# Kernel optimization log

Hardware: AMD Instinct MI355X
Metric: run time of the kernel (lower is better)

## Reference

```python
import jax, jax.numpy as jnp
import numpy as np

N_RAYS = 16384
MAX_HITS = 16
S_PER_VOX = 4          # samples per intersected voxel
N_VOX = 524288         # voxel embedding table size
D_VOX = 16             # voxel feature dim
HID = 64               # sdf/rgb MLP hidden dim
FEAT = 15              # geometry feature dim passed to rgb net
BETA = 0.1             # VolSDF-style laplace/logistic density sharpness


def setup_inputs() -> dict:
    key = jax.random.key(0)
    ks = jax.random.split(key, 12)
    rays_o = jax.random.normal(ks[0], (N_RAYS, 3), dtype=jnp.float32)
    rd = jax.random.normal(ks[1], (N_RAYS, 3), dtype=jnp.float32)
    rays_d = rd / jnp.linalg.norm(rd, axis=-1, keepdims=True)
    raw = jax.random.randint(ks[2], (N_RAYS, MAX_HITS), 0, 2 * N_VOX)
    vox_idx = jnp.where(raw < N_VOX, raw, -1)
    t0 = jnp.sort(jax.random.uniform(ks[3], (N_RAYS, MAX_HITS), minval=0.5, maxval=6.0), axis=-1)
    seg = jax.random.uniform(ks[4], (N_RAYS, MAX_HITS), minval=0.02, maxval=0.2)
    t_near, t_far = t0, t0 + seg
    ray_hits = jnp.any(vox_idx >= 0, axis=-1)
    s = 0.1
    embed_table = jax.random.normal(ks[5], (N_VOX, D_VOX), dtype=jnp.float32) * s
    W1 = jax.random.normal(ks[6], (3 + D_VOX, HID), dtype=jnp.float32) * s
    b1 = jnp.zeros((HID,), jnp.float32)
    W2 = jax.random.normal(ks[7], (HID, 1 + FEAT), dtype=jnp.float32) * s
    b2 = jnp.zeros((1 + FEAT,), jnp.float32)
    Wr1 = jax.random.normal(ks[8], (3 + FEAT, HID), dtype=jnp.float32) * s
    br1 = jnp.zeros((HID,), jnp.float32)
    Wr2 = jax.random.normal(ks[9], (HID, 3), dtype=jnp.float32) * s
    br2 = jnp.zeros((3,), jnp.float32)
    return dict(rays_o=rays_o, rays_d=rays_d, vox_idx=vox_idx, t_near=t_near,
                t_far=t_far, ray_hits=ray_hits, embed_table=embed_table,
                W1=W1, b1=b1, W2=W2, b2=b2, Wr1=Wr1, br1=br1, Wr2=Wr2, br2=br2)


def reference(rays_o, rays_d, vox_idx, t_near, t_far, ray_hits,
              embed_table, W1, b1, W2, b2, Wr1, br1, Wr2, br2):
    N = rays_o.shape[0]
    M = MAX_HITS * S_PER_VOX  # max_samples per ray
    # ---- point_sampler: S_PER_VOX uniform midpoints inside each hit voxel ----
    frac = (jnp.arange(S_PER_VOX, dtype=jnp.float32) + 0.5) / S_PER_VOX  # [S]
    seg = t_far - t_near                                                  # [N,H]
    t_vals = (t_near[..., None] + seg[..., None] * frac).reshape(N, M)    # [N,M]
    dists = jnp.broadcast_to((seg / S_PER_VOX)[..., None],
                             (N, MAX_HITS, S_PER_VOX)).reshape(N, M)      # [N,M]
    p2v_idx = jnp.broadcast_to(vox_idx[..., None],
                               (N, MAX_HITS, S_PER_VOX)).reshape(N, M)    # [N,M]
    mask_pts = p2v_idx >= 0                                               # [N,M]
    pts = rays_o[:, None, :] + t_vals[..., None] * rays_d[:, None, :]     # [N,M,3]
    # ---- voxel_embedder: gather voxel features (safe-index the misses) ----
    safe_idx = jnp.where(mask_pts, p2v_idx, 0)
    vox_embeds = embed_table[safe_idx]                                    # [N,M,Dv]
    # ---- sdf_net: 2-layer MLP -> sdf (1) + geometry feats (FEAT) ----
    x = jnp.concatenate([pts, vox_embeds], axis=-1)
    h = jax.nn.relu(jnp.einsum('nmi,ih->nmh', x, W1) + b1)
    so = jnp.einsum('nmh,ho->nmo', h, W2) + b2
    sdf = so[..., 0]                                                      # [N,M]
    feats = so[..., 1:]                                                   # [N,M,FEAT]
    # ---- rgb_net on (view dir, feats) ----
    rdir = jnp.broadcast_to(rays_d[:, None, :], (N, M, 3))
    xr = jnp.concatenate([rdir, feats], axis=-1)
    hr = jax.nn.relu(jnp.einsum('nmi,ih->nmh', xr, Wr1) + br1)
    rgb = jax.nn.sigmoid(jnp.einsum('nmh,ho->nmo', hr, Wr2) + br2)        # [N,M,3]
    # ---- density_fn + masked_scatter (invalid points -> 0) ----
    density = (1.0 / BETA) * jax.nn.sigmoid(-sdf / BETA)
    mf = mask_pts.astype(rgb.dtype)
    free_energy = density * dists * mf                                    # [N,M]
    rgb = rgb * mf[..., None]
    sdf_sc = sdf * mf
    # ---- volumetric_rendering_sdf ----
    alpha = 1.0 - jnp.exp(-free_energy)
    shifted = jnp.concatenate([jnp.zeros_like(free_energy[:, :1]),
                               jnp.cumsum(free_energy, axis=-1)[:, :-1]], axis=-1)
    T = jnp.exp(-shifted)
    weights = alpha * T                                                   # [N,M]
    rgb_map = jnp.einsum('nm,nmc->nc', weights, rgb)                      # [N,3]
    depth = jnp.sum(weights * t_vals, axis=-1)
    acc = jnp.sum(weights, axis=-1)
    eps = 1e-10
    disp = 1.0 / jnp.maximum(eps, depth / jnp.maximum(acc, eps))
    # ---- fill_in for rays with no hits (eval path) ----
    hm = ray_hits
    rgb_map = jnp.where(hm[:, None], rgb_map, 0.0)
    depth = jnp.where(hm, depth, 0.0)
    disp = jnp.where(hm, disp, 1000.0)
    acc = jnp.where(hm, acc, 0.0)
    weights = jnp.where(hm[:, None], weights, 0.0)
    sdf_out = jnp.where(hm[:, None], sdf_sc, 1.0)
    return rgb_map, depth, disp, acc, weights, sdf_out
```

## Files before the change

### kernel.cpp

```cpp
#include <hip/hip_runtime.h>

#define NRAYS  16384
#define WPB    4
#define GRID   4096

typedef _Float16 f16x2 __attribute__((ext_vector_type(2)));
typedef _Float16 f16x4 __attribute__((ext_vector_type(4)));
typedef _Float16 f16x8 __attribute__((ext_vector_type(8)));
typedef float    f32x4 __attribute__((ext_vector_type(4)));

static __device__ __forceinline__ f16x2 pk(float a, float b) {
    return __builtin_bit_cast(f16x2, __builtin_amdgcn_cvt_pkrtz(a, b));
}
static __device__ __forceinline__ f16x4 cat2(f16x2 lo, f16x2 hi) {
    return __builtin_shufflevector(lo, hi, 0, 1, 2, 3);
}
static __device__ __forceinline__ f16x4 pack4relu(f32x4 v) {
    f16x4 p = cat2(pk(v[0], v[1]), pk(v[2], v[3]));
    return __builtin_elementwise_max(p, (f16x4){});
}
template <int CTRL, int RMASK>
static __device__ __forceinline__ float dppadd(float x) {
    int t = __builtin_amdgcn_update_dpp(0, __builtin_bit_cast(int, x), CTRL, RMASK, 0xf, true);
    return x + __builtin_bit_cast(float, t);
}
static __device__ __forceinline__ float wavescan(float x) {
    x = dppadd<0x111, 0xf>(x);
    x = dppadd<0x112, 0xf>(x);
    x = dppadd<0x114, 0xf>(x);
    x = dppadd<0x118, 0xf>(x);
    x = dppadd<0x142, 0xa>(x);
    x = dppadd<0x143, 0xc>(x);
    return x;
}
static __device__ __forceinline__ float lane63(float x) {
    return __builtin_bit_cast(float, __builtin_amdgcn_readlane(__builtin_bit_cast(int, x), 63));
}
static __device__ __forceinline__ _Float16* rowp(_Float16* b, int row, int ch) {
    return b + (row << 5) + ((ch ^ (row & 3)) << 3);
}

#define MFMA32(a, b, c) __builtin_amdgcn_mfma_f32_16x16x32_f16(a, b, c, 0, 0, 0)
#define MFMA16(a, b, c) __builtin_amdgcn_mfma_f32_16x16x16f16(a, b, c, 0, 0, 0)

extern "C" __global__ void prep_frags(
    const float* __restrict__ W1, const float* __restrict__ b1,
    const float* __restrict__ W2, const float* __restrict__ b2,
    const float* __restrict__ Wr1, const float* __restrict__ br1,
    const float* __restrict__ Wr2, const float* __restrict__ br2,
    void* __restrict__ ws)
{
    _Float16* wsh = (_Float16*)ws;
    float*    wsf = (float*)ws;
    const int b = blockIdx.x;
    const int tid = threadIdx.x;
    const int l = tid & 63, g = tid >> 6;
    const int c = l & 15, q = l >> 4;
    if (b == 0) {
        const int m = g;
        #pragma unroll
        for (int e = 0; e < 8; ++e) {
            const int k = q * 8 + e;
            const float v = (k < 19) ? W1[k * 64 + m * 16 + c]
                                     : (k == 19 ? b1[m * 16 + c] : 0.f);
            wsh[(m * 64 + l) * 8 + e] = (_Float16)v;
        }
    } else if (b == 1) {
        const int mh = g;
        #pragma unroll
        for (int e = 0; e < 4; ++e) {
            wsh[2048 + (mh * 64 + l) * 4 + e] = (_Float16)W2[(mh * 16 + q * 4 + e) * 16 + c];
            wsh[5120 + (mh * 64 + l) * 4 + e] =
                (c < 3) ? (_Float16)Wr2[(mh * 16 + q * 4 + e) * 3 + c] : (_Float16)0.f;
        }
    } else if (b == 2) {
        const int mh = g;
        #pragma unroll
        for (int ks = 0; ks < 2; ++ks)
            #pragma unroll
            for (int e = 0; e < 4; ++e) {
                const int k = ks * 16 + q * 4 + e;
                const float v = (k < 18) ? Wr1[k * 64 + mh * 16 + c]
                                         : (k == 18 ? br1[mh * 16 + c] : 0.f);
                wsh[3072 + ((mh * 2 + ks) * 64 + l) * 4 + e] = (_Float16)v;
            }
    } else {
        if (g == 0) {
            #pragma unroll
            for (int j = 0; j < 4; ++j) wsf[3072 + l * 4 + j] = b2[q * 4 + j];
        } else if (g == 1) {
            #pragma unroll
            for (int j = 0; j < 4; ++j)
                wsf[3328 + l * 4 + j] = ((q * 4 + j) < 3) ? br2[q * 4 + j] : 0.f;
        }
    }
}

extern "C" __global__ __launch_bounds__(256, 4) void nerf_render_mfma(
    const float* __restrict__ rays_o,
    const float* __restrict__ rays_d,
    const int*   __restrict__ vox_idx,
    const float* __restrict__ t_near,
    const float* __restrict__ t_far,
    const float* __restrict__ embed,
    const void*  __restrict__ ws,
    float* __restrict__ out)
{
    __shared__ __align__(16) _Float16 buf_all[WPB][64 * 32];
    __shared__ __align__(16) f32x4    hof_all[WPB][64];
    __shared__ float                  sdf_all[WPB][64];

    const _Float16* frag  = (const _Float16*)ws;
    const float*    fragf = (const float*)ws;

    const int lane = threadIdx.x & 63;
    const int wv   = threadIdx.x >> 6;
    _Float16* buf = buf_all[wv];
    f32x4* hof = hof_all[wv];
    float* sdfb = sdf_all[wv];

    const int c  = lane & 15;
    const int q  = lane >> 4;
    const bool q0 = (q == 0);
    const int hh = lane >> 2, ss = lane & 3;
    const int bpaddr = ((lane + 48) & 63) << 2;

    const int ray = blockIdx.x * WPB + wv;

    const int   vi_raw = vox_idx[ray * 16 + hh];
    const float tn  = t_near[ray * 16 + hh];
    const float tfv = t_far [ray * 16 + hh];
    const float ox = rays_o[ray*3+0], oy = rays_o[ray*3+1], oz = rays_o[ray*3+2];
    const float dx = rays_d[ray*3+0], dy = rays_d[ray*3+1], dz = rays_d[ray*3+2];
    const int vi0 = vi_raw >= 0 ? vi_raw : 0;
    const float4* er = reinterpret_cast<const float4*>(embed + (long long)vi0 * 16);
    const float4 e0 = er[0], e1 = er[1], e2 = er[2], e3 = er[3];

    *(f16x8*)rowp(buf, lane, 3) = (f16x8){};

    const bool  mask = vi_raw >= 0;
    const float seg  = tfv - tn;
    const float t    = fmaf(seg, ((float)ss + 0.5f) * 0.25f, tn);
    const float dist = seg * 0.25f;
    const float p0 = fmaf(t, dx, ox), p1 = fmaf(t, dy, oy), p2 = fmaf(t, dz, oz);

    f16x8 r0 = {(_Float16)p0,   (_Float16)p1,   (_Float16)p2,   (_Float16)e0.x,
                (_Float16)e0.y, (_Float16)e0.z, (_Float16)e0.w, (_Float16)e1.x};
    f16x8 r1 = {(_Float16)e1.y, (_Float16)e1.z, (_Float16)e1.w, (_Float16)e2.x,
                (_Float16)e2.y, (_Float16)e2.z, (_Float16)e2.w, (_Float16)e3.x};
    f16x8 r2 = {(_Float16)e3.y, (_Float16)e3.z, (_Float16)e3.w, (_Float16)1.0f,
                (_Float16)0.0f, (_Float16)0.0f, (_Float16)0.0f, (_Float16)0.0f};
    *(f16x8*)rowp(buf, lane, 0) = r0;
    *(f16x8*)rowp(buf, lane, 1) = r1;
    *(f16x8*)rowp(buf, lane, 2) = r2;

    f16x8 bx[4];
    #pragma unroll
    for (int n = 0; n < 4; ++n)
        bx[n] = *(const f16x8*)rowp(buf, n * 16 + c, q);

    const f32x4 b2v = *(const f32x4*)(fragf + 3072 + lane * 4);
    f32x4 acc2[4];
    #pragma unroll
    for (int n = 0; n < 4; ++n) acc2[n] = b2v;
    #pragma unroll 1
    for (int m = 0; m < 4; ++m) {
        const f16x8 w1f = *(const f16x8*)(frag + (m * 64 + lane) * 8);
        const f16x4 w2a = *(const f16x4*)(frag + 2048 + (m * 64 + lane) * 4);
        #pragma unroll
        for (int np = 0; np < 2; ++np) {
            f32x4 a1[2] = {};
            #pragma unroll
            for (int i = 0; i < 2; ++i) a1[i] = MFMA32(w1f, bx[np * 2 + i], a1[i]);
            #pragma unroll
            for (int i = 0; i < 2; ++i) {
                const f16x4 hb = pack4relu(a1[i]);
                acc2[np * 2 + i] = MFMA16(w2a, hb, acc2[np * 2 + i]);
            }
        }
    }

    float sdfv[4]; f16x2 d0[4], d1[4]; int bd[4];
    #pragma unroll
    for (int n = 0; n < 4; ++n) {
        sdfv[n] = acc2[n][0];
        d0[n] = pk(acc2[n][0], acc2[n][1]);
        d1[n] = pk(acc2[n][2], acc2[n][3]);
    }
    #pragma unroll
    for (int n = 0; n < 4; ++n)
        bd[n] = __builtin_amdgcn_ds_bpermute(bpaddr, __builtin_bit_cast(int, d1[n]));

    if (q0) {
        #pragma unroll
        for (int n = 0; n < 4; ++n) sdfb[n * 16 + c] = sdfv[n];
    }

    const f16x2 dir01 = pk(dx, dy);
    const _Float16 dzh = (_Float16)dz;
    const f16x2 zero2 = {};
    const f16x2 onezero = {(_Float16)1.0f, (_Float16)0.0f};
    f16x4 bfr0[4], bfr1[4];
    #pragma unroll
    for (int n = 0; n < 4; ++n) {
        f16x2 bdn = __builtin_bit_cast(f16x2, bd[n]);
        f16x2 lo0 = q0 ? dir01 : bdn;
        f16x2 hi0 = q0 ? (f16x2){dzh, d0[n][1]} : d0[n];
        bfr0[n] = cat2(lo0, hi0);
        f16x2 lo1 = q0 ? bdn : zero2;
        f16x2 hi1 = q0 ? onezero : zero2;
        bfr1[n] = cat2(lo1, hi1);
    }

    float* out_rgb   = out;
    float* out_depth = out + NRAYS * 3;
    float* out_disp  = out_depth + NRAYS;
    float* out_acc   = out_disp + NRAYS;
    float* out_w     = out_acc + NRAYS;
    float* out_sdf   = out_w + NRAYS * 64;

    const float sdfs = sdfb[lane];
    const float mf = mask ? 1.0f : 0.0f;
    const float density = 10.0f / (1.0f + __expf(10.0f * sdfs));
    const float fe      = density * dist * mf;
    const float sdf_sc  = sdfs * mf;

    const float cum   = wavescan(fe);
    const float T     = __expf(fe - cum);
    const float alpha = 1.0f - __expf(-fe);
    const float w     = alpha * T;

    const float swt = lane63(wavescan(w * t));
    const float swa = lane63(wavescan(w));

    const bool hm = (__ballot((int)mask) != 0ull);

    out_w  [ray * 64 + lane] = hm ? w      : 0.0f;
    out_sdf[ray * 64 + lane] = hm ? sdf_sc : 1.0f;
    if (lane == 0) {
        if (hm) {
            out_depth[ray] = swt;
            out_acc[ray]   = swa;
            const float dd = swt / fmaxf(swa, 1e-10f);
            out_disp[ray]  = 1.0f / fmaxf(1e-10f, dd);
        } else {
            out_depth[ray] = 0.0f;
            out_acc[ray]   = 0.0f;
            out_disp[ray]  = 1000.0f;
        }
    }

    const f32x4 br2v = *(const f32x4*)(fragf + 3328 + lane * 4);
    f32x4 acc4[4];
    #pragma unroll
    for (int n = 0; n < 4; ++n) acc4[n] = br2v;
    #pragma unroll 1
    for (int mh = 0; mh < 4; ++mh) {
        const f16x4 wa0 = *(const f16x4*)(frag + 3072 + ((mh * 2 + 0) * 64 + lane) * 4);
        const f16x4 wa1 = *(const f16x4*)(frag + 3072 + ((mh * 2 + 1) * 64 + lane) * 4);
        const f16x4 w4  = *(const f16x4*)(frag + 5120 + (mh * 64 + lane) * 4);
        #pragma unroll
        for (int np = 0; np < 2; ++np) {
            f32x4 a3[2] = {};
            #pragma unroll
            for (int i = 0; i < 2; ++i) a3[i] = MFMA16(wa0, bfr0[np * 2 + i], a3[i]);
            #pragma unroll
            for (int i = 0; i < 2; ++i) a3[i] = MFMA16(wa1, bfr1[np * 2 + i], a3[i]);
            #pragma unroll
            for (int i = 0; i < 2; ++i) {
                const f16x4 hr = pack4relu(a3[i]);
                acc4[np * 2 + i] = MFMA16(w4, hr, acc4[np * 2 + i]);
            }
        }
    }

    if (q0) {
        #pragma unroll
        for (int n = 0; n < 4; ++n) {
            f32x4 o4 = {acc4[n][0], acc4[n][1], acc4[n][2], 0.0f};
            hof[n * 16 + c] = o4;
        }
    }
    const f32x4 mine = hof[lane];

    const float rr = mf / (1.0f + __expf(-mine[0]));
    const float gg = mf / (1.0f + __expf(-mine[1]));
    const float bb = mf / (1.0f + __expf(-mine[2]));

    const float swr = lane63(wavescan(w * rr));
    const float swg = lane63(wavescan(w * gg));
    const float swb = lane63(wavescan(w * bb));

    if (lane == 0) {
        if (hm) {
            out_rgb[ray * 3 + 0] = swr;
            out_rgb[ray * 3 + 1] = swg;
            out_rgb[ray * 3 + 2] = swb;
        } else {
            out_rgb[ray * 3 + 0] = 0.0f;
            out_rgb[ray * 3 + 1] = 0.0f;
            out_rgb[ray * 3 + 2] = 0.0f;
        }
    }
}

extern "C" void kernel_launch(void* const* d_in, const int* in_sizes, int n_in,
                              void* d_out, int out_size, void* d_ws, size_t ws_size,
                              hipStream_t stream) {
    const float* rays_o = (const float*)d_in[0];
    const float* rays_d = (const float*)d_in[1];
    const int*   vox    = (const int*)  d_in[2];
    const float* t_near = (const float*)d_in[3];
    const float* t_far  = (const float*)d_in[4];
    const float* embed  = (const float*)d_in[6];
    const float* W1  = (const float*)d_in[7];
    const float* b1  = (const float*)d_in[8];
    const float* W2  = (const float*)d_in[9];
    const float* b2  = (const float*)d_in[10];
    const float* Wr1 = (const float*)d_in[11];
    const float* br1 = (const float*)d_in[12];
    const float* Wr2 = (const float*)d_in[13];
    const float* br2 = (const float*)d_in[14];
    float* outp = (float*)d_out;

    prep_frags<<<dim3(4), dim3(256), 0, stream>>>(W1, b1, W2, b2, Wr1, br1, Wr2, br2, d_ws);
    nerf_render_mfma<<<dim3(GRID), dim3(256), 0, stream>>>(rays_o, rays_d, vox, t_near, t_far,
                                                           embed, d_ws, outp);
}
```

Measured before the change: 31.40 us.

## Split MLP passes into half-batches and alias LDS to double occupancy

```diff
diff --git a/kernel.cpp b/kernel.cpp
--- a/kernel.cpp
+++ b/kernel.cpp
@@ -96,7 +96,7 @@
     }
 }
 
-extern "C" __global__ __launch_bounds__(256, 4) void nerf_render_mfma(
+extern "C" __global__ __launch_bounds__(256, 8) void nerf_render_mfma(
     const float* __restrict__ rays_o,
     const float* __restrict__ rays_d,
     const int*   __restrict__ vox_idx,
@@ -107,8 +107,6 @@
     float* __restrict__ out)
 {
     __shared__ __align__(16) _Float16 buf_all[WPB][64 * 32];
-    __shared__ __align__(16) f32x4    hof_all[WPB][64];
-    __shared__ float                  sdf_all[WPB][64];
 
     const _Float16* frag  = (const _Float16*)ws;
     const float*    fragf = (const float*)ws;
@@ -116,8 +114,8 @@
     const int lane = threadIdx.x & 63;
     const int wv   = threadIdx.x >> 6;
     _Float16* buf = buf_all[wv];
-    f32x4* hof = hof_all[wv];
-    float* sdfb = sdf_all[wv];
+    f32x4* hof  = reinterpret_cast<f32x4*>(buf);
+    float* sdfb = reinterpret_cast<float*>(buf + 512);
 
     const int c  = lane & 15;
     const int q  = lane >> 4;
@@ -143,6 +141,9 @@
     const float t    = fmaf(seg, ((float)ss + 0.5f) * 0.25f, tn);
     const float dist = seg * 0.25f;
     const float p0 = fmaf(t, dx, ox), p1 = fmaf(t, dy, oy), p2 = fmaf(t, dz, oz);
+
+    const f16x2 dir01 = pk(dx, dy);
+    const _Float16 dzh = (_Float16)dz;
 
     f16x8 r0 = {(_Float16)p0,   (_Float16)p1,   (_Float16)p2,   (_Float16)e0.x,
                 (_Float16)e0.y, (_Float16)e0.z, (_Float16)e0.w, (_Float16)e1.x};
@@ -154,62 +155,42 @@
     *(f16x8*)rowp(buf, lane, 1) = r1;
     *(f16x8*)rowp(buf, lane, 2) = r2;
 
-    f16x8 bx[4];
-    #pragma unroll
-    for (int n = 0; n < 4; ++n)
-        bx[n] = *(const f16x8*)rowp(buf, n * 16 + c, q);
-
     const f32x4 b2v = *(const f32x4*)(fragf + 3072 + lane * 4);
-    f32x4 acc2[4];
-    #pragma unroll
-    for (int n = 0; n < 4; ++n) acc2[n] = b2v;
-    #pragma unroll 1
-    for (int m = 0; m < 4; ++m) {
-        const f16x8 w1f = *(const f16x8*)(frag + (m * 64 + lane) * 8);
-        const f16x4 w2a = *(const f16x4*)(frag + 2048 + (m * 64 + lane) * 4);
-        #pragma unroll
-        for (int np = 0; np < 2; ++np) {
-            f32x4 a1[2] = {};
-            #pragma unroll
-            for (int i = 0; i < 2; ++i) a1[i] = MFMA32(w1f, bx[np * 2 + i], a1[i]);
-            #pragma unroll
-            for (int i = 0; i < 2; ++i) {
-                const f16x4 hb = pack4relu(a1[i]);
-                acc2[np * 2 + i] = MFMA16(w2a, hb, acc2[np * 2 + i]);
-            }
-        }
-    }
-
-    float sdfv[4]; f16x2 d0[4], d1[4]; int bd[4];
-    #pragma unroll
-    for (int n = 0; n < 4; ++n) {
-        sdfv[n] = acc2[n][0];
-        d0[n] = pk(acc2[n][0], acc2[n][1]);
-        d1[n] = pk(acc2[n][2], acc2[n][3]);
-    }
-    #pragma unroll
-    for (int n = 0; n < 4; ++n)
-        bd[n] = __builtin_amdgcn_ds_bpermute(bpaddr, __builtin_bit_cast(int, d1[n]));
+    f32x4 acc20 = b2v, acc21 = b2v, acc22 = b2v, acc23 = b2v;
+    {
+        const f16x8 bx0 = *(const f16x8*)rowp(buf,      c, q);
+        const f16x8 bx1 = *(const f16x8*)rowp(buf, 16 + c, q);
+        #pragma unroll 1
+        for (int m = 0; m < 4; ++m) {
+            const f16x8 w1f = *(const f16x8*)(frag + (m * 64 + lane) * 8);
+            const f16x4 w2a = *(const f16x4*)(frag + 2048 + (m * 64 + lane) * 4);
+            f32x4 a10 = {}, a11 = {};
+            a10 = MFMA32(w1f, bx0, a10);
+            a11 = MFMA32(w1f, bx1, a11);
+            acc20 = MFMA16(w2a, pack4relu(a10), acc20);
+            acc21 = MFMA16(w2a, pack4relu(a11), acc21);
+        }
+    }
+    {
+        const f16x8 bx2 = *(const f16x8*)rowp(buf, 32 + c, q);
+        const f16x8 bx3 = *(const f16x8*)rowp(buf, 48 + c, q);
+        #pragma unroll 1
+        for (int m = 0; m < 4; ++m) {
+            const f16x8 w1f = *(const f16x8*)(frag + (m * 64 + lane) * 8);
+            const f16x4 w2a = *(const f16x4*)(frag + 2048 + (m * 64 + lane) * 4);
+            f32x4 a12 = {}, a13 = {};
+            a12 = MFMA32(w1f, bx2, a12);
+            a13 = MFMA32(w1f, bx3, a13);
+            acc22 = MFMA16(w2a, pack4relu(a12), acc22);
+            acc23 = MFMA16(w2a, pack4relu(a13), acc23);
+        }
+    }
 
     if (q0) {
-        #pragma unroll
-        for (int n = 0; n < 4; ++n) sdfb[n * 16 + c] = sdfv[n];
-    }
-
-    const f16x2 dir01 = pk(dx, dy);
-    const _Float16 dzh = (_Float16)dz;
-    const f16x2 zero2 = {};
-    const f16x2 onezero = {(_Float16)1.0f, (_Float16)0.0f};
-    f16x4 bfr0[4], bfr1[4];
-    #pragma unroll
-    for (int n = 0; n < 4; ++n) {
-        f16x2 bdn = __builtin_bit_cast(f16x2, bd[n]);
-        f16x2 lo0 = q0 ? dir01 : bdn;
-        f16x2 hi0 = q0 ? (f16x2){dzh, d0[n][1]} : d0[n];
-        bfr0[n] = cat2(lo0, hi0);
-        f16x2 lo1 = q0 ? bdn : zero2;
-        f16x2 hi1 = q0 ? onezero : zero2;
-        bfr1[n] = cat2(lo1, hi1);
+        sdfb[     c] = acc20[0];
+        sdfb[16 + c] = acc21[0];
+        sdfb[32 + c] = acc22[0];
+        sdfb[48 + c] = acc23[0];
     }
 
     float* out_rgb   = out;
@@ -251,38 +232,73 @@
     }
 
     const f32x4 br2v = *(const f32x4*)(fragf + 3328 + lane * 4);
-    f32x4 acc4[4];
-    #pragma unroll
-    for (int n = 0; n < 4; ++n) acc4[n] = br2v;
-    #pragma unroll 1
-    for (int mh = 0; mh < 4; ++mh) {
-        const f16x4 wa0 = *(const f16x4*)(frag + 3072 + ((mh * 2 + 0) * 64 + lane) * 4);
-        const f16x4 wa1 = *(const f16x4*)(frag + 3072 + ((mh * 2 + 1) * 64 + lane) * 4);
-        const f16x4 w4  = *(const f16x4*)(frag + 5120 + (mh * 64 + lane) * 4);
-        #pragma unroll
-        for (int np = 0; np < 2; ++np) {
-            f32x4 a3[2] = {};
-            #pragma unroll
-            for (int i = 0; i < 2; ++i) a3[i] = MFMA16(wa0, bfr0[np * 2 + i], a3[i]);
-            #pragma unroll
-            for (int i = 0; i < 2; ++i) a3[i] = MFMA16(wa1, bfr1[np * 2 + i], a3[i]);
-            #pragma unroll
-            for (int i = 0; i < 2; ++i) {
-                const f16x4 hr = pack4relu(a3[i]);
-                acc4[np * 2 + i] = MFMA16(w4, hr, acc4[np * 2 + i]);
-            }
-        }
-    }
-
-    if (q0) {
-        #pragma unroll
-        for (int n = 0; n < 4; ++n) {
-            f32x4 o4 = {acc4[n][0], acc4[n][1], acc4[n][2], 0.0f};
-            hof[n * 16 + c] = o4;
-        }
-    }
+    const f16x2 zero2 = {};
+    const f16x2 onezero = {(_Float16)1.0f, (_Float16)0.0f};
+
+    {
+        const f16x2 d00 = pk(acc20[0], acc20[1]), d10 = pk(acc20[2], acc20[3]);
+        const f16x2 d01 = pk(acc21[0], acc21[1]), d11 = pk(acc21[2], acc21[3]);
+        const f16x2 bd0 = __builtin_bit_cast(f16x2,
+            __builtin_amdgcn_ds_bpermute(bpaddr, __builtin_bit_cast(int, d10)));
+        const f16x2 bd1 = __builtin_bit_cast(f16x2,
+            __builtin_amdgcn_ds_bpermute(bpaddr, __builtin_bit_cast(int, d11)));
+        const f16x4 bfr00 = cat2(q0 ? dir01 : bd0, q0 ? (f16x2){dzh, d00[1]} : d00);
+        const f16x4 bfr01 = cat2(q0 ? dir01 : bd1, q0 ? (f16x2){dzh, d01[1]} : d01);
+        const f16x4 bfr10 = cat2(q0 ? bd0 : zero2, q0 ? onezero : zero2);
+        const f16x4 bfr11 = cat2(q0 ? bd1 : zero2, q0 ? onezero : zero2);
+
+        f32x4 acc40 = br2v, acc41 = br2v;
+        #pragma unroll 1
+        for (int mh = 0; mh < 4; ++mh) {
+            const f16x4 wa0 = *(const f16x4*)(frag + 3072 + ((mh * 2 + 0) * 64 + lane) * 4);
+            const f16x4 wa1 = *(const f16x4*)(frag + 3072 + ((mh * 2 + 1) * 64 + lane) * 4);
+            const f16x4 w4  = *(const f16x4*)(frag + 5120 + (mh * 64 + lane) * 4);
+            f32x4 a30 = {}, a31 = {};
+            a30 = MFMA16(wa0, bfr00, a30);
+            a31 = MFMA16(wa0, bfr01, a31);
+            a30 = MFMA16(wa1, bfr10, a30);
+            a31 = MFMA16(wa1, bfr11, a31);
+            acc40 = MFMA16(w4, pack4relu(a30), acc40);
+            acc41 = MFMA16(w4, pack4relu(a31), acc41);
+        }
+        if (q0) {
+            hof[     c] = (f32x4){acc40[0], acc40[1], acc40[2], 0.0f};
+            hof[16 + c] = (f32x4){acc41[0], acc41[1], acc41[2], 0.0f};
+        }
+    }
+    {
+        const f16x2 d02 = pk(acc22[0], acc22[1]), d12 = pk(acc22[2], acc22[3]);
+        const f16x2 d03 = pk(acc23[0], acc23[1]), d13 = pk(acc23[2], acc23[3]);
+        const f16x2 bd2 = __builtin_bit_cast(f16x2,
+            __builtin_amdgcn_ds_bpermute(bpaddr, __builtin_bit_cast(int, d12)));
+        const f16x2 bd3 = __builtin_bit_cast(f16x2,
+            __builtin_amdgcn_ds_bpermute(bpaddr, __builtin_bit_cast(int, d13)));
+        const f16x4 bfr02 = cat2(q0 ? dir01 : bd2, q0 ? (f16x2){dzh, d02[1]} : d02);
+        const f16x4 bfr03 = cat2(q0 ? dir01 : bd3, q0 ? (f16x2){dzh, d03[1]} : d03);
+        const f16x4 bfr12 = cat2(q0 ? bd2 : zero2, q0 ? onezero : zero2);
+        const f16x4 bfr13 = cat2(q0 ? bd3 : zero2, q0 ? onezero : zero2);
+
+        f32x4 acc42 = br2v, acc43 = br2v;
+        #pragma unroll 1
+        for (int mh = 0; mh < 4; ++mh) {
+            const f16x4 wa0 = *(const f16x4*)(frag + 3072 + ((mh * 2 + 0) * 64 + lane) * 4);
+            const f16x4 wa1 = *(const f16x4*)(frag + 3072 + ((mh * 2 + 1) * 64 + lane) * 4);
+            const f16x4 w4  = *(const f16x4*)(frag + 5120 + (mh * 64 + lane) * 4);
+            f32x4 a32 = {}, a33 = {};
+            a32 = MFMA16(wa0, bfr02, a32);
+            a33 = MFMA16(wa0, bfr03, a33);
+            a32 = MFMA16(wa1, bfr12, a32);
+            a33 = MFMA16(wa1, bfr13, a33);
+            acc42 = MFMA16(w4, pack4relu(a32), acc42);
+            acc43 = MFMA16(w4, pack4relu(a33), acc43);
+        }
+        if (q0) {
+            hof[32 + c] = (f32x4){acc42[0], acc42[1], acc42[2], 0.0f};
+            hof[48 + c] = (f32x4){acc43[0], acc43[1], acc43[2], 0.0f};
+        }
+    }
+
     const f32x4 mine = hof[lane];
-
     const float rr = mf / (1.0f + __expf(-mine[0]));
     const float gg = mf / (1.0f + __expf(-mine[1]));
     const float bb = mf / (1.0f + __expf(-mine[2]));
```

New measurement: 35.97 us. 14.5% more time.
